# Optimization experiments

Measured on AMD Instinct MI355X. Metric: run time of the kernel, lower is better.

Reference implementation:

```python
import jax, jax.numpy as jnp
import numpy as np

BETA = 5.5
ALPHA = 0.5

def _l2norm(x, eps=1e-12):
    # matches torch F.normalize(dim=-1): x / max(||x||, eps)
    n = jnp.sqrt(jnp.sum(x * x, axis=-1, keepdims=True))
    return x / jnp.maximum(n, eps)

def setup_inputs() -> dict:
    key = jax.random.key(0)
    k1, k2 = jax.random.split(key)
    query_features = jax.random.normal(k1, (4096, 512), dtype=jnp.float32)
    support_keys = jax.random.normal(k2, (16384, 512), dtype=jnp.float32)
    return {"query_features": query_features, "support_keys": support_keys}

def reference(query_features, support_keys):
    cache_keys = _l2norm(support_keys)              # (N, D)
    q = _l2norm(query_features)                     # (B, D)
    affinity = jnp.einsum('bd,nd->bn', q, cache_keys)   # (B, N) cosine sims
    affinity = jnp.exp(-BETA * (1.0 - affinity))
    retrieved = jnp.einsum('bn,nd->bd', affinity, cache_keys)  # (B, D)
    return query_features + ALPHA * retrieved
```

## Files before the change

### kernel.cpp

```cpp
#include <hip/hip_runtime.h>
#include <cstdint>
#include <cstddef>

#define BETA 5.5f
#define ALPHA 0.5f

constexpr int D   = 512;
constexpr int NB  = 4096;
constexpr int NK  = 16384;
constexpr int BQ  = 64;
constexpr int BN  = 64;
constexpr int NSPLIT = 4;
constexpr int NRANGE = NK / NSPLIT;
constexpr int CHUNKS = NRANGE / BN;
constexpr int KROW = D + 8;
constexpr int PROW = BN + 8;

typedef __attribute__((ext_vector_type(8)))  short    short8;
typedef __attribute__((ext_vector_type(4)))  float    floatx4;
typedef __attribute__((ext_vector_type(4)))  uint32_t uint4v;
typedef __attribute__((ext_vector_type(2)))  uint32_t uint2v;

__device__ inline uint32_t f2bf1(float f) {
  union { float f; uint32_t u; } v; v.f = f;
  return (v.u + 0x7FFFu + ((v.u >> 16) & 1u)) >> 16;
}
__device__ inline uint32_t pack2(float a, float b) {
  return f2bf1(a) | (f2bf1(b) << 16);
}

__device__ inline void load_lds16(const void* g, void* l) {
  __builtin_amdgcn_global_load_lds(
      (const __attribute__((address_space(1))) uint32_t*)g,
      (__attribute__((address_space(3))) uint32_t*)l, 16, 0, 0);
}

__global__ void norm_q_kernel(const float* __restrict__ q,
                              float* __restrict__ out,
                              unsigned short* __restrict__ Qn) {
  const int wave = threadIdx.x >> 6, lane = threadIdx.x & 63;
  const int row = blockIdx.x * 4 + wave;
  const float4* qr = (const float4*)(q + (size_t)row * D);
  float4 a = qr[lane * 2];
  float4 b = qr[lane * 2 + 1];
  float ss = a.x*a.x + a.y*a.y + a.z*a.z + a.w*a.w
           + b.x*b.x + b.y*b.y + b.z*b.z + b.w*b.w;
#pragma unroll
  for (int m = 32; m >= 1; m >>= 1) ss += __shfl_xor(ss, m, 64);
  const float sc = 1.0f / fmaxf(sqrtf(ss), 1e-12f);
  float4* orow = (float4*)(out + (size_t)row * D);
  orow[lane * 2]     = a;
  orow[lane * 2 + 1] = b;
  uint4v w;
  w.x = pack2(a.x*sc, a.y*sc); w.y = pack2(a.z*sc, a.w*sc);
  w.z = pack2(b.x*sc, b.y*sc); w.w = pack2(b.z*sc, b.w*sc);
  *(uint4v*)(Qn + (size_t)row * D + lane * 8) = w;
}

__global__ void norm_k_kernel(const float* __restrict__ k,
                              unsigned short* __restrict__ Kn,
                              unsigned short* __restrict__ KnT) {
  __shared__ unsigned short tile[64 * KROW];
  const int wave = threadIdx.x >> 6, lane = threadIdx.x & 63;
  const int n0 = blockIdx.x * 64;
#pragma unroll
  for (int i = 0; i < 4; ++i) {
    const int rl = wave * 4 + i;
    const int n  = n0 + rl;
    const float4* kr = (const float4*)(k + (size_t)n * D);
    float4 a = kr[lane * 2], b = kr[lane * 2 + 1];
    float ss = a.x*a.x + a.y*a.y + a.z*a.z + a.w*a.w
             + b.x*b.x + b.y*b.y + b.z*b.z + b.w*b.w;
#pragma unroll
    for (int m = 32; m >= 1; m >>= 1) ss += __shfl_xor(ss, m, 64);
    const float sc = 1.0f / fmaxf(sqrtf(ss), 1e-12f);
    uint4v w;
    w.x = pack2(a.x*sc, a.y*sc); w.y = pack2(a.z*sc, a.w*sc);
    w.z = pack2(b.x*sc, b.y*sc); w.w = pack2(b.z*sc, b.w*sc);
    *(uint4v*)(Kn + (size_t)n * D + lane * 8) = w;
    *(uint4v*)&tile[rl * KROW + lane * 8]     = w;
  }
  __syncthreads();
  const int dsub = threadIdx.x >> 3;
  const int nl   = (threadIdx.x & 7) * 8;
#pragma unroll
  for (int iter = 0; iter < 4; ++iter) {
    const int d = iter * 128 + dsub;
    uint4v w;
    w.x = (uint32_t)tile[(nl+0)*KROW + d] | ((uint32_t)tile[(nl+1)*KROW + d] << 16);
    w.y = (uint32_t)tile[(nl+2)*KROW + d] | ((uint32_t)tile[(nl+3)*KROW + d] << 16);
    w.z = (uint32_t)tile[(nl+4)*KROW + d] | ((uint32_t)tile[(nl+5)*KROW + d] << 16);
    w.w = (uint32_t)tile[(nl+6)*KROW + d] | ((uint32_t)tile[(nl+7)*KROW + d] << 16);
    *(uint4v*)(KnT + (size_t)d * NK + n0 + nl) = w;
  }
}

__global__ __launch_bounds__(512, 2) void fused_kernel(
    const unsigned short* __restrict__ Qn,
    const unsigned short* __restrict__ Kn,
    const unsigned short* __restrict__ KnT,
    float* __restrict__ out) {
  __shared__ unsigned short K_lds[2][BN * KROW];
  __shared__ unsigned short P_lds[2][BQ * PROW];

  const int tid  = threadIdx.x;
  const int wave = tid >> 6, lane = tid & 63;
  const int l15  = lane & 15, quad = lane >> 4;
  const int nsplit = blockIdx.x & (NSPLIT - 1);
  const int qtile  = blockIdx.x >> 2;
  const int q0     = qtile * BQ;
  const int nbase  = nsplit * NRANGE;
  const int tb = wave & 3, nh = wave >> 2;

  short8 qf[16];
  {
    const unsigned short* qrow = Qn + (size_t)(q0 + tb * 16 + l15) * D + quad * 8;
#pragma unroll
    for (int kb = 0; kb < 16; ++kb) qf[kb] = *(const short8*)(qrow + kb * 32);
  }

  floatx4 oacc[4][4] = {};
  short8 ktf[2][4];

  const unsigned short* ktrow = KnT + (size_t)(wave*64 + l15) * NK + nbase + quad*8;

  auto stage = [&](int ch, int buf) {
#pragma unroll
    for (int i = 0; i < 8; ++i) {
      const int row = wave * 8 + i;
      load_lds16(Kn + (size_t)(nbase + ch*BN + row) * D + lane * 8,
                 &K_lds[buf][row * KROW]);
    }
  };
  auto ktf_load_h = [&](int ch, int kb2) {
#pragma unroll
    for (int td = 0; td < 4; ++td)
      ktf[kb2][td] = *(const short8*)(ktrow + (size_t)td*16*NK + ch*BN + kb2*32);
  };
  auto pf_read = [&](int pbuf, int kb2, short8* pf) {
#pragma unroll
    for (int tr = 0; tr < 4; ++tr)
      pf[tr] = *(const short8*)&P_lds[pbuf][(tr*16 + l15) * PROW + kb2*32 + quad*8];
  };
  auto gemm2_mfma = [&](const short8* pf, const short8* kt) {
#pragma unroll
    for (int td = 0; td < 4; ++td)
#pragma unroll
      for (int tr = 0; tr < 4; ++tr)
        oacc[tr][td] = __builtin_amdgcn_mfma_f32_16x16x32_bf16(
            pf[tr], kt[td], oacc[tr][td], 0, 0, 0);
  };
  auto a_read4 = [&](int buf, int kb0, short8* af) {
#pragma unroll
    for (int i = 0; i < 4; ++i) {
      af[2*i]   = *(const short8*)&K_lds[buf][(nh*32 +      l15) * KROW + (kb0+i)*32 + quad*8];
      af[2*i+1] = *(const short8*)&K_lds[buf][(nh*32 + 16 + l15) * KROW + (kb0+i)*32 + quad*8];
    }
  };
  auto gemm1_mfma4 = [&](const short8* af, int kb0, floatx4& s0, floatx4& s1) {
#pragma unroll
    for (int i = 0; i < 4; ++i) {
      s0 = __builtin_amdgcn_mfma_f32_16x16x32_bf16(af[2*i],   qf[kb0+i], s0, 0, 0, 0);
      s1 = __builtin_amdgcn_mfma_f32_16x16x32_bf16(af[2*i+1], qf[kb0+i], s1, 0, 0, 0);
    }
  };
  auto exp_pw = [&](int buf, const floatx4& s0, const floatx4& s1) {
    const int prow = (tb * 16 + l15) * PROW;
    uint2v w0, w1;
    w0.x = pack2(__expf(BETA * (s0[0] - 1.f)), __expf(BETA * (s0[1] - 1.f)));
    w0.y = pack2(__expf(BETA * (s0[2] - 1.f)), __expf(BETA * (s0[3] - 1.f)));
    w1.x = pack2(__expf(BETA * (s1[0] - 1.f)), __expf(BETA * (s1[1] - 1.f)));
    w1.y = pack2(__expf(BETA * (s1[2] - 1.f)), __expf(BETA * (s1[3] - 1.f)));
    *(uint2v*)&P_lds[buf][prow + (nh*2 + 0) * 16 + quad * 4] = w0;
    *(uint2v*)&P_lds[buf][prow + (nh*2 + 1) * 16 + quad * 4] = w1;
  };
  auto ph = [&]() {
    asm volatile("s_barrier" ::: "memory");
    asm volatile("s_waitcnt lgkmcnt(0)" ::: "memory");
    __builtin_amdgcn_s_setprio(1);
  };
  auto ph_done = [&]() { __builtin_amdgcn_s_setprio(0); };

  stage(0, 0);
  ktf_load_h(0, 0); ktf_load_h(0, 1);
  asm volatile("s_waitcnt vmcnt(8)" ::: "memory");
  asm volatile("s_barrier" ::: "memory");
  {
    stage(1, 1);
    floatx4 s0 = {0.f,0.f,0.f,0.f}, s1 = {0.f,0.f,0.f,0.f};
    short8 af[8];
#pragma unroll
    for (int g = 0; g < 4; ++g) {
      a_read4(0, g*4, af);
      gemm1_mfma4(af, g*4, s0, s1);
    }
    exp_pw(0, s0, s1);
  }
  asm volatile("s_waitcnt vmcnt(0) lgkmcnt(0)" ::: "memory");
  asm volatile("s_barrier" ::: "memory");

#pragma unroll 1
  for (int c = 0; c + 2 < CHUNKS; ++c) {
    const int cur = c & 1, nxt = cur ^ 1;
    floatx4 s0 = {0.f,0.f,0.f,0.f}, s1 = {0.f,0.f,0.f,0.f};
    short8 pf[4], af[8];
    stage(c + 2, cur);
    pf_read(cur, 0, pf);
    ph(); gemm2_mfma(pf, ktf[0]); ph_done();
    a_read4(nxt, 0, af);
    ph(); gemm1_mfma4(af, 0, s0, s1); ph_done();
    a_read4(nxt, 4, af);
    ph(); gemm1_mfma4(af, 4, s0, s1); ph_done();
    pf_read(cur, 1, pf);
    ktf_load_h(c + 1, 0);
    ph(); gemm2_mfma(pf, ktf[1]); ph_done();
    a_read4(nxt, 8, af);
    ktf_load_h(c + 1, 1);
    ph(); gemm1_mfma4(af, 8, s0, s1); ph_done();
    a_read4(nxt, 12, af);
    ph(); gemm1_mfma4(af, 12, s0, s1); ph_done();
    exp_pw(nxt, s0, s1);
    asm volatile("s_waitcnt vmcnt(8) lgkmcnt(0)" ::: "memory");
    asm volatile("s_barrier" ::: "memory");
  }
  {
    const int c = CHUNKS - 2, cur = c & 1, nxt = cur ^ 1;
    floatx4 s0 = {0.f,0.f,0.f,0.f}, s1 = {0.f,0.f,0.f,0.f};
    short8 pf[4], af[8];
    pf_read(cur, 0, pf);
    ph(); gemm2_mfma(pf, ktf[0]); ph_done();
    a_read4(nxt, 0, af);
    ph(); gemm1_mfma4(af, 0, s0, s1); ph_done();
    a_read4(nxt, 4, af);
    ph(); gemm1_mfma4(af, 4, s0, s1); ph_done();
    pf_read(cur, 1, pf);
    ktf_load_h(CHUNKS - 1, 0);
    ph(); gemm2_mfma(pf, ktf[1]); ph_done();
    a_read4(nxt, 8, af);
    ktf_load_h(CHUNKS - 1, 1);
    ph(); gemm1_mfma4(af, 8, s0, s1); ph_done();
    a_read4(nxt, 12, af);
    ph(); gemm1_mfma4(af, 12, s0, s1); ph_done();
    exp_pw(nxt, s0, s1);
    asm volatile("s_waitcnt lgkmcnt(0)" ::: "memory");
    asm volatile("s_barrier" ::: "memory");
  }
  {
    const int cur = (CHUNKS - 1) & 1;
    short8 pf[4];
    pf_read(cur, 0, pf);
    gemm2_mfma(pf, ktf[0]);
    pf_read(cur, 1, pf);
    gemm2_mfma(pf, ktf[1]);
  }

  const int colbase = wave * 64 + l15;
#pragma unroll
  for (int tr = 0; tr < 4; ++tr)
#pragma unroll
    for (int td = 0; td < 4; ++td)
#pragma unroll
      for (int r = 0; r < 4; ++r)
        atomicAdd(out + (size_t)(q0 + tr*16 + quad*4 + r) * D + colbase + td*16,
                  ALPHA * oacc[tr][td][r]);
}

extern "C" void kernel_launch(void* const* d_in, const int* in_sizes, int n_in,
                              void* d_out, int out_size, void* d_ws, size_t ws_size,
                              hipStream_t stream) {
  (void)in_sizes; (void)n_in; (void)out_size; (void)ws_size;
  const float* q = (const float*)d_in[0];
  const float* k = (const float*)d_in[1];
  float* out = (float*)d_out;
  unsigned short* Qn  = (unsigned short*)d_ws;
  unsigned short* Kn  = Qn + (size_t)NB * D;
  unsigned short* KnT = Kn + (size_t)NK * D;

  hipLaunchKernelGGL(norm_q_kernel, dim3(NB / 4),  dim3(256),  0, stream, q, out, Qn);
  hipLaunchKernelGGL(norm_k_kernel, dim3(NK / 64), dim3(1024), 0, stream, k, Kn, KnT);
  hipLaunchKernelGGL(fused_kernel, dim3((NB / BQ) * NSPLIT), dim3(512), 0, stream,
                     Qn, Kn, KnT, out);
}
```

Before: 318.6 us.

## Remove per-phase barriers and double-buffer LDS fragment reads to overlap with MFMA

Result: faster. 280.1 us (-12.1%).

```diff
diff --git a/kernel.cpp b/kernel.cpp
--- a/kernel.cpp
+++ b/kernel.cpp
@@ -143,12 +143,14 @@
       pf[tr] = *(const short8*)&P_lds[pbuf][(tr*16 + l15) * PROW + kb2*32 + quad*8];
   };
   auto gemm2_mfma = [&](const short8* pf, const short8* kt) {
+    __builtin_amdgcn_s_setprio(1);
 #pragma unroll
     for (int td = 0; td < 4; ++td)
 #pragma unroll
       for (int tr = 0; tr < 4; ++tr)
         oacc[tr][td] = __builtin_amdgcn_mfma_f32_16x16x32_bf16(
             pf[tr], kt[td], oacc[tr][td], 0, 0, 0);
+    __builtin_amdgcn_s_setprio(0);
   };
   auto a_read4 = [&](int buf, int kb0, short8* af) {
 #pragma unroll
@@ -158,11 +160,13 @@
     }
   };
   auto gemm1_mfma4 = [&](const short8* af, int kb0, floatx4& s0, floatx4& s1) {
+    __builtin_amdgcn_s_setprio(1);
 #pragma unroll
     for (int i = 0; i < 4; ++i) {
       s0 = __builtin_amdgcn_mfma_f32_16x16x32_bf16(af[2*i],   qf[kb0+i], s0, 0, 0, 0);
       s1 = __builtin_amdgcn_mfma_f32_16x16x32_bf16(af[2*i+1], qf[kb0+i], s1, 0, 0, 0);
     }
+    __builtin_amdgcn_s_setprio(0);
   };
   auto exp_pw = [&](int buf, const floatx4& s0, const floatx4& s1) {
     const int prow = (tb * 16 + l15) * PROW;
@@ -174,12 +178,6 @@
     *(uint2v*)&P_lds[buf][prow + (nh*2 + 0) * 16 + quad * 4] = w0;
     *(uint2v*)&P_lds[buf][prow + (nh*2 + 1) * 16 + quad * 4] = w1;
   };
-  auto ph = [&]() {
-    asm volatile("s_barrier" ::: "memory");
-    asm volatile("s_waitcnt lgkmcnt(0)" ::: "memory");
-    __builtin_amdgcn_s_setprio(1);
-  };
-  auto ph_done = [&]() { __builtin_amdgcn_s_setprio(0); };
 
   stage(0, 0);
   ktf_load_h(0, 0); ktf_load_h(0, 1);
@@ -188,12 +186,15 @@
   {
     stage(1, 1);
     floatx4 s0 = {0.f,0.f,0.f,0.f}, s1 = {0.f,0.f,0.f,0.f};
-    short8 af[8];
-#pragma unroll
-    for (int g = 0; g < 4; ++g) {
-      a_read4(0, g*4, af);
-      gemm1_mfma4(af, g*4, s0, s1);
-    }
+    short8 afA[8], afB[8];
+    a_read4(0, 0, afA);
+    a_read4(0, 4, afB);
+    gemm1_mfma4(afA, 0, s0, s1);
+    a_read4(0, 8, afA);
+    gemm1_mfma4(afB, 4, s0, s1);
+    a_read4(0, 12, afB);
+    gemm1_mfma4(afA, 8, s0, s1);
+    gemm1_mfma4(afB, 12, s0, s1);
     exp_pw(0, s0, s1);
   }
   asm volatile("s_waitcnt vmcnt(0) lgkmcnt(0)" ::: "memory");
@@ -203,55 +204,55 @@
   for (int c = 0; c + 2 < CHUNKS; ++c) {
     const int cur = c & 1, nxt = cur ^ 1;
     floatx4 s0 = {0.f,0.f,0.f,0.f}, s1 = {0.f,0.f,0.f,0.f};
-    short8 pf[4], af[8];
+    short8 pf0[4], pf1[4], afA[8], afB[8];
     stage(c + 2, cur);
-    pf_read(cur, 0, pf);
-    ph(); gemm2_mfma(pf, ktf[0]); ph_done();
-    a_read4(nxt, 0, af);
-    ph(); gemm1_mfma4(af, 0, s0, s1); ph_done();
-    a_read4(nxt, 4, af);
-    ph(); gemm1_mfma4(af, 4, s0, s1); ph_done();
-    pf_read(cur, 1, pf);
+    pf_read(cur, 0, pf0);
+    a_read4(nxt, 0, afA);
+    gemm2_mfma(pf0, ktf[0]);
+    a_read4(nxt, 4, afB);
+    gemm1_mfma4(afA, 0, s0, s1);
+    pf_read(cur, 1, pf1);
+    gemm1_mfma4(afB, 4, s0, s1);
+    a_read4(nxt, 8, afA);
     ktf_load_h(c + 1, 0);
-    ph(); gemm2_mfma(pf, ktf[1]); ph_done();
-    a_read4(nxt, 8, af);
+    gemm2_mfma(pf1, ktf[1]);
+    a_read4(nxt, 12, afB);
     ktf_load_h(c + 1, 1);
-    ph(); gemm1_mfma4(af, 8, s0, s1); ph_done();
-    a_read4(nxt, 12, af);
-    ph(); gemm1_mfma4(af, 12, s0, s1); ph_done();
+    gemm1_mfma4(afA, 8, s0, s1);
+    gemm1_mfma4(afB, 12, s0, s1);
     exp_pw(nxt, s0, s1);
     asm volatile("s_waitcnt vmcnt(8) lgkmcnt(0)" ::: "memory");
     asm volatile("s_barrier" ::: "memory");
   }
   {
-    const int c = CHUNKS - 2, cur = c & 1, nxt = cur ^ 1;
+    const int cur = (CHUNKS - 2) & 1, nxt = cur ^ 1;
     floatx4 s0 = {0.f,0.f,0.f,0.f}, s1 = {0.f,0.f,0.f,0.f};
-    short8 pf[4], af[8];
-    pf_read(cur, 0, pf);
-    ph(); gemm2_mfma(pf, ktf[0]); ph_done();
-    a_read4(nxt, 0, af);
-    ph(); gemm1_mfma4(af, 0, s0, s1); ph_done();
-    a_read4(nxt, 4, af);
-    ph(); gemm1_mfma4(af, 4, s0, s1); ph_done();
-    pf_read(cur, 1, pf);
+    short8 pf0[4], pf1[4], afA[8], afB[8];
+    pf_read(cur, 0, pf0);
+    a_read4(nxt, 0, afA);
+    gemm2_mfma(pf0, ktf[0]);
+    a_read4(nxt, 4, afB);
+    gemm1_mfma4(afA, 0, s0, s1);
+    pf_read(cur, 1, pf1);
+    gemm1_mfma4(afB, 4, s0, s1);
+    a_read4(nxt, 8, afA);
     ktf_load_h(CHUNKS - 1, 0);
-    ph(); gemm2_mfma(pf, ktf[1]); ph_done();
-    a_read4(nxt, 8, af);
+    gemm2_mfma(pf1, ktf[1]);
+    a_read4(nxt, 12, afB);
     ktf_load_h(CHUNKS - 1, 1);
-    ph(); gemm1_mfma4(af, 8, s0, s1); ph_done();
-    a_read4(nxt, 12, af);
-    ph(); gemm1_mfma4(af, 12, s0, s1); ph_done();
+    gemm1_mfma4(afA, 8, s0, s1);
+    gemm1_mfma4(afB, 12, s0, s1);
     exp_pw(nxt, s0, s1);
     asm volatile("s_waitcnt lgkmcnt(0)" ::: "memory");
     asm volatile("s_barrier" ::: "memory");
   }
   {
     const int cur = (CHUNKS - 1) & 1;
-    short8 pf[4];
-    pf_read(cur, 0, pf);
-    gemm2_mfma(pf, ktf[0]);
-    pf_read(cur, 1, pf);
-    gemm2_mfma(pf, ktf[1]);
+    short8 pf0[4], pf1[4];
+    pf_read(cur, 0, pf0);
+    pf_read(cur, 1, pf1);
+    gemm2_mfma(pf0, ktf[0]);
+    gemm2_mfma(pf1, ktf[1]);
   }
 
   const int colbase = wave * 64 + l15;
```
